# Kernel tuning notes

Measured on AMD Instinct MI355X. Metric: run time of the kernel, lower is better.

Reference implementation:

```python
import jax, jax.numpy as jnp
from jax import lax
import numpy as np

NUM_HEADS = 8
PATCH = 16
EPS_SUM = 1e-6


def resize_nearest(x, H, W):
    # torch F.interpolate(mode='nearest'): src = floor(dst * in / out)
    ih, iw = x.shape[-2], x.shape[-1]
    ri = (jnp.arange(H) * ih) // H
    ci = (jnp.arange(W) * iw) // W
    return x[:, :, ri][:, :, :, ci]


def single_scale(x, delta, wq, bq, ws, bs):
    # x: [1+K, C, H, W]; delta: [K, 1, H0, W0]
    q, s = x[:1], x[1:]
    K, C, H, W = s.shape
    d = C // NUM_HEADS
    P = PATCH
    Hp, Wp = H // P, W // P
    S = P * P
    delta = resize_nearest(delta, H, W)  # [K,1,H,W]

    qf = jnp.transpose(q, (0, 2, 3, 1))[0] @ wq.T + bq            # [H,W,C]
    qh = qf.reshape(H, W, NUM_HEADS, d).transpose(2, 0, 1, 3)     # [h,H,W,d]
    sf = jnp.transpose(s, (0, 2, 3, 1)) @ ws.T + bs               # [K,H,W,C]
    sh = sf.reshape(K, H, W, NUM_HEADS, d).transpose(0, 3, 1, 2, 4)  # [K,h,H,W,d]

    fg = delta.reshape(K, P, Hp, P, Wp).transpose(0, 1, 3, 2, 4).reshape(K, S, Hp * Wp)
    bg = 1.0 - fg
    fg_sum = jnp.maximum(fg.sum(-1), EPS_SUM)  # [K,S]
    bg_sum = jnp.maximum(bg.sum(-1), EPS_SUM)

    sp = sh.reshape(K, NUM_HEADS, P, Hp, P, Wp, d).transpose(0, 1, 2, 4, 3, 5, 6)
    sp = sp.reshape(K, NUM_HEADS, S, Hp * Wp, d)  # [K,h,S,l,d]

    c_fg = jnp.einsum('ksl,khsld->khsd', fg, sp) / fg_sum[:, None, :, None]
    c_bg = jnp.einsum('ksl,khsld->khsd', bg, sp) / bg_sum[:, None, :, None]
    # concat along prototype dim then flatten as [h, K*2S, d] (K-major, fg-then-bg)
    c_s = jnp.concatenate([c_fg, c_bg], axis=2).transpose(1, 0, 2, 3).reshape(NUM_HEADS, K * 2 * S, d)
    v = jnp.concatenate([jnp.ones((K, S), c_s.dtype), jnp.zeros((K, S), c_s.dtype)], axis=1).reshape(-1)  # [K*2S]

    mask = jnp.concatenate([
        jnp.where(fg_sum < 1.0, -jnp.inf, 0.0),
        jnp.where(bg_sum < 1.0, -jnp.inf, 0.0)], axis=1).reshape(-1)  # [K*2S]

    attn = jnp.einsum('hyxd,hsd->hyxs', qh, c_s) + mask  # [h,H,W,K*2S]
    attn = jax.nn.softmax(attn, axis=-1)
    out = jnp.einsum('hyxs,s->hyx', attn, v)  # [h,H,W]
    return out.mean(0)[None, None]  # [1,1,H,W]


def group_norm(x, gamma, beta, groups=4, eps=1e-5):
    N, C, H, W = x.shape
    xr = x.reshape(N, groups, C // groups, H, W)
    mu = xr.mean((2, 3, 4), keepdims=True)
    var = xr.var((2, 3, 4), keepdims=True)
    xr = (xr - mu) * lax.rsqrt(var + eps)
    return xr.reshape(N, C, H, W) * gamma[None, :, None, None] + beta[None, :, None, None]


def conv2d(x, w, b, pad):
    y = lax.conv_general_dilated(x, w, (1, 1), [(pad, pad), (pad, pad)],
                                 dimension_numbers=('NCHW', 'OIHW', 'NCHW'))
    return y + b[None, :, None, None]


def setup_inputs() -> dict:
    key = jax.random.key(0)
    ks = jax.random.split(key, 24)
    K, C, H, W = 5, 256, 64, 64
    inp = {}
    for i in range(4):
        inp[f'x{i}'] = jax.random.normal(ks[i], (1 + K, C, H, W), jnp.float32)
    inp['delta_onehot_x'] = jax.random.randint(ks[4], (K, 1, 256, 256), 0, 2).astype(jnp.float32)
    inp['wq'] = jax.random.normal(ks[5], (C, C), jnp.float32) * 0.02
    inp['bq'] = jnp.zeros((C,), jnp.float32)
    inp['ws'] = jax.random.normal(ks[6], (C, C), jnp.float32) * 0.02
    inp['bs'] = jnp.zeros((C,), jnp.float32)
    inp['cw1'] = jax.random.normal(ks[7], (16, 4, 5, 5), jnp.float32) * 0.05
    inp['cb1'] = jnp.zeros((16,), jnp.float32)
    inp['g1'] = jnp.ones((16,), jnp.float32)
    inp['be1'] = jnp.zeros((16,), jnp.float32)
    inp['cw2'] = jax.random.normal(ks[8], (64, 16, 5, 5), jnp.float32) * 0.05
    inp['cb2'] = jnp.zeros((64,), jnp.float32)
    inp['g2'] = jnp.ones((64,), jnp.float32)
    inp['be2'] = jnp.zeros((64,), jnp.float32)
    inp['cw3'] = jax.random.normal(ks[9], (128, 64, 3, 3), jnp.float32) * 0.05
    inp['cb3'] = jnp.zeros((128,), jnp.float32)
    inp['g3'] = jnp.ones((128,), jnp.float32)
    inp['be3'] = jnp.zeros((128,), jnp.float32)
    return inp


def reference(x0, x1, x2, x3, delta_onehot_x, wq, bq, ws, bs,
              cw1, cb1, g1, be1, cw2, cb2, g2, be2, cw3, cb3, g3, be3):
    masks = [single_scale(x, delta_onehot_x, wq, bq, ws, bs) for x in (x0, x1, x2, x3)]
    cm = jnp.concatenate(masks, axis=1)  # [1, nlayers=4, H, W]
    # idx=1 conv head: kernels [5,5,3], channels [16,64,128], GroupNorm(4)+ReLU
    h = jax.nn.relu(group_norm(conv2d(cm, cw1, cb1, 2), g1, be1))
    h = jax.nn.relu(group_norm(conv2d(h, cw2, cb2, 2), g2, be2))
    h = jax.nn.relu(group_norm(conv2d(h, cw3, cb3, 1), g3, be3))
    return h
```

## Files before the change

kernel.cpp:

```cpp
#include <hip/hip_runtime.h>
#include <hip/hip_bf16.h>
#include <stdint.h>

#define CCH 256
#define NPIX 4096
#define NH 8
#define M2 2560
#define LOG2E 1.44269504088896f
#define GN_NB 32

typedef __attribute__((ext_vector_type(8))) short short8;
typedef __attribute__((ext_vector_type(4))) float f32x4;

__device__ __forceinline__ uint16_t f2bfu(float f) {
    uint32_t u = __builtin_bit_cast(uint32_t, f);
    return (uint16_t)((u + 0x7FFFu + ((u >> 16) & 1u)) >> 16);
}
__device__ __forceinline__ uint32_t pack_bf2(float a, float b) {
    return (uint32_t)f2bfu(a) | ((uint32_t)f2bfu(b) << 16);
}
__device__ __forceinline__ short8 u4_to_s8(uint4 v) {
    return __builtin_bit_cast(short8, v);
}

__device__ __forceinline__ void prep_w_one(const float* __restrict__ w, uint16_t* __restrict__ Wk,
                                           int idx, int Cin, int Cout, int K2) {
    int kk = idx & 31;
    int oc = (idx >> 5) % Cout;
    int ck = idx / (32 * Cout);
    int k = ck * 32 + kk;
    int tap = k / Cin, ic = k % Cin;
    float v = (tap < K2) ? w[((size_t)oc * Cin + ic) * K2 + tap] : 0.0f;
    Wk[idx] = f2bfu(v);
}

__global__ void prep_all(const float* __restrict__ wq, const float* __restrict__ wsm,
                         const float* __restrict__ cw1, const float* __restrict__ cw2,
                         const float* __restrict__ cw3,
                         uint16_t* __restrict__ WB, uint16_t* __restrict__ Wk1,
                         uint16_t* __restrict__ Wk2, uint16_t* __restrict__ Wk3) {
    int idx = blockIdx.x * 256 + threadIdx.x;
    if (idx < 131072) {
        const float* src = (idx < 65536) ? wq : wsm;
        WB[idx] = f2bfu(src[idx & 65535]);
        return;
    }
    idx -= 131072;
    if (idx < 2048)  { prep_w_one(cw1, Wk1, idx, 4, 16, 25);  return; }
    idx -= 2048;
    if (idx < 26624) { prep_w_one(cw2, Wk2, idx, 16, 64, 25); return; }
    idx -= 26624;
    if (idx < 73728) { prep_w_one(cw3, Wk3, idx, 64, 128, 9); return; }
}

__global__ __launch_bounds__(256) void patch_sum(
        const float* __restrict__ x0, const float* __restrict__ x1,
        const float* __restrict__ x2, const float* __restrict__ x3,
        const float* __restrict__ dox, uint16_t* __restrict__ PS,
        float* __restrict__ inv, float* __restrict__ mexpb) {
    int z = blockIdx.z;
    int sc = z / 5, k = z % 5;
    const float* xim = ((sc == 0) ? x0 : (sc == 1) ? x1 : (sc == 2) ? x2 : x3)
                       + (size_t)(k + 1) * CCH * NPIX;
    int p1 = blockIdx.x, chq = blockIdx.y;
    int tid = threadIdx.x;
    int cloc = tid >> 6, col = tid & 63;
    __shared__ float wls[4][64];
    __shared__ uint16_t pst[2][16][72];
    wls[cloc][col] = dox[(size_t)k * 65536 + (size_t)(16 * p1 + 4 * cloc) * 256 + 4 * col];
    __syncthreads();
    float w0 = wls[0][col], w1 = wls[1][col], w2 = wls[2][col], w3 = wls[3][col];
    const float* xbase = xim + p1 * 256 + col;
#pragma unroll 4
    for (int it = 0; it < 16; ++it) {
        int c = chq * 64 + it * 4 + cloc;
        const float* xp = xbase + (size_t)c * NPIX;
        float v0 = xp[0], v1 = xp[64], v2 = xp[128], v3 = xp[192];
        float pf = w0 * v0 + w1 * v1 + w2 * v2 + w3 * v3;
        float pb = (v0 + v1 + v2 + v3) - pf;
        pf += __shfl_xor(pf, 1); pf += __shfl_xor(pf, 2);
        pb += __shfl_xor(pb, 1); pb += __shfl_xor(pb, 2);
        if ((col & 3) == 0) {
            int q = col >> 2, cl = it * 4 + cloc;
            pst[0][q][cl] = f2bfu(pf);
            pst[1][q][cl] = f2bfu(pb);
        }
    }
    if (chq == 0 && tid < 64) {
        float ws = w0 + w1 + w2 + w3;
        ws += __shfl_xor(ws, 1); ws += __shfl_xor(ws, 2);
        if ((col & 3) == 0) {
            int s = p1 * 16 + (col >> 2);
            float fsum = ws, bsum = 16.f - ws;
            int mf = k * 512 + s, mbk = mf + 256;
            mexpb[sc * M2 + mf]  = (fsum < 1.f) ? 0.f : 1.f;
            mexpb[sc * M2 + mbk] = (bsum < 1.f) ? 0.f : 1.f;
            inv[(size_t)(z * 2 + 0) * 256 + s] = 1.f / fmaxf(fsum, 1e-6f);
            inv[(size_t)(z * 2 + 1) * 256 + s] = 1.f / fmaxf(bsum, 1e-6f);
        }
    }
    __syncthreads();
    int fb = tid >> 7, rem = tid & 127;
    int q = rem >> 3, chunk = rem & 7;
    uint4 v = *(const uint4*)&pst[fb][q][chunk * 8];
    int s = p1 * 16 + q;
    *(uint4*)&PS[((size_t)(z * 2 + fb) * 256 + s) * CCH + chq * 64 + chunk * 8] = v;
}

__global__ __launch_bounds__(256) void cent_gemm(
        const uint16_t* __restrict__ PS, const uint16_t* __restrict__ WB,
        const float* __restrict__ bs, const float* __restrict__ inv,
        uint16_t* __restrict__ Csbf) {
    int tid = threadIdx.x, lane = tid & 63, wid = tid >> 6;
    int lp = lane & 15, g = lane >> 4;
    int rowb = blockIdx.x * 128 + wid * 32;
    int cob = blockIdx.y * 64;
    const uint16_t* wsb = WB + 65536;
    f32x4 acc[2][4] = {};
#pragma unroll
    for (int ks = 0; ks < 8; ++ks) {
        int k0 = ks * 32;
        uint4 a0 = *(const uint4*)(PS + (size_t)(rowb + lp) * CCH + k0 + g * 8);
        uint4 a1 = *(const uint4*)(PS + (size_t)(rowb + 16 + lp) * CCH + k0 + g * 8);
        short8 af[2] = {u4_to_s8(a0), u4_to_s8(a1)};
        short8 b[4];
#pragma unroll
        for (int t = 0; t < 4; ++t) {
            uint4 bw = *(const uint4*)(wsb + (size_t)(cob + t * 16 + lp) * 256 + k0 + g * 8);
            b[t] = u4_to_s8(bw);
        }
#pragma unroll
        for (int m = 0; m < 2; ++m)
#pragma unroll
            for (int t = 0; t < 4; ++t)
                acc[m][t] = __builtin_amdgcn_mfma_f32_16x16x32_bf16(af[m], b[t], acc[m][t], 0, 0, 0);
    }
#pragma unroll
    for (int m = 0; m < 2; ++m)
#pragma unroll
        for (int t = 0; t < 4; ++t) {
            int co = cob + t * 16 + lp;
            int h = co >> 5, d = co & 31;
            float bv = bs[co];
#pragma unroll
            for (int r = 0; r < 4; ++r) {
                int row = rowb + m * 16 + g * 4 + r;
                int zz = row >> 9, fb = (row >> 8) & 1, s = row & 255;
                int scc = zz / 5, kk = zz % 5;
                int slot = kk * 512 + fb * 256 + s;
                float val = acc[m][t][r] * inv[row] + bv;
                Csbf[(((size_t)scc * NH + h) * M2 + slot) * 32 + d] = f2bfu(val);
            }
        }
}

__global__ __launch_bounds__(512) void q_gemm(
        const float* __restrict__ x0, const float* __restrict__ x1,
        const float* __restrict__ x2, const float* __restrict__ x3,
        const uint16_t* __restrict__ WB, const float* __restrict__ bq,
        uint16_t* __restrict__ Qbf) {
    int sc = blockIdx.y;
    const float* xim = (sc == 0) ? x0 : (sc == 1) ? x1 : (sc == 2) ? x2 : x3;
    int p0 = blockIdx.x * 64;
    int tid = threadIdx.x, lane = tid & 63, wid = tid >> 6;
    int lp = lane & 15, g = lane >> 4;
    int wm = wid >> 1, wn = wid & 1;
    __shared__ uint32_t Al[16][68];
    f32x4 acc[8] = {};
#pragma unroll
    for (int ks = 0; ks < 8; ++ks) {
        int k0 = ks * 32;
        __syncthreads();
        if (tid < 256) {
            int rp = tid >> 4, f4i = tid & 15;
            float4 v0 = *(const float4*)(xim + (size_t)(k0 + 2 * rp) * NPIX + p0 + f4i * 4);
            float4 v1 = *(const float4*)(xim + (size_t)(k0 + 2 * rp + 1) * NPIX + p0 + f4i * 4);
            *(uint4*)&Al[rp][f4i * 4] = make_uint4(
                pack_bf2(v0.x, v1.x), pack_bf2(v0.y, v1.y),
                pack_bf2(v0.z, v1.z), pack_bf2(v0.w, v1.w));
        }
        __syncthreads();
        short8 b[8];
#pragma unroll
        for (int tn = 0; tn < 8; ++tn) {
            uint4 bw = *(const uint4*)(WB + (size_t)(wn * 128 + tn * 16 + lp) * 256 + k0 + g * 8);
            b[tn] = u4_to_s8(bw);
        }
        int px = wm * 16 + lp;
        uint4 av = make_uint4(Al[4 * g + 0][px], Al[4 * g + 1][px],
                              Al[4 * g + 2][px], Al[4 * g + 3][px]);
        short8 af = u4_to_s8(av);
#pragma unroll
        for (int tn = 0; tn < 8; ++tn)
            acc[tn] = __builtin_amdgcn_mfma_f32_16x16x32_bf16(af, b[tn], acc[tn], 0, 0, 0);
    }
#pragma unroll
    for (int tn = 0; tn < 8; ++tn) {
        int co = wn * 128 + tn * 16 + lp;
        float bv = bq[co];
#pragma unroll
        for (int r = 0; r < 4; ++r) {
            int row = p0 + wm * 16 + g * 4 + r;
            Qbf[((size_t)(sc * NPIX + row)) * CCH + co] = f2bfu((acc[tn][r] + bv) * LOG2E);
        }
    }
}

__global__ __launch_bounds__(256) void attn_v6(
        const uint16_t* __restrict__ Qbf, const uint16_t* __restrict__ Csbf,
        const float* __restrict__ mexpb, float* __restrict__ sfbuf) {
    int head = blockIdx.y;
    int sc = blockIdx.z >> 2, split = blockIdx.z & 3;
    int tid = threadIdx.x;
    int lane = tid & 63, wid = tid >> 6;
    int lp = lane & 15, g = lane >> 4;
    int p0w = blockIdx.x * 256 + wid * 64;

    const uint16_t* Qs = Qbf + (size_t)sc * NPIX * CCH;
    const uint16_t* csb = Csbf + ((size_t)sc * NH + head) * M2 * 32;
    const float* mb = mexpb + sc * M2;

    short8 aq[4];
#pragma unroll
    for (int m = 0; m < 4; m++) {
        uint4 qv = *(const uint4*)(Qs + (size_t)(p0w + m * 16 + lp) * CCH + head * 32 + g * 8);
        aq[m] = u4_to_s8(qv);
    }

    const f32x4 zero4 = {0.f, 0.f, 0.f, 0.f};
    float sfg[4][4] = {}, sbg[4][4] = {};
    int cbeg = split * 640;
    for (int c0loc = 0; c0loc < 640; c0loc += 64) {
        int c0 = cbeg + c0loc;
        bool fg = ((c0 & 511) < 256);
        short8 bf[4];
        float mexp[4];
#pragma unroll
        for (int t = 0; t < 4; t++) {
            int row = c0 + t * 16 + lp;
            bf[t] = u4_to_s8(*(const uint4*)(csb + (size_t)row * 32 + g * 8));
            mexp[t] = mb[row];
        }
        if (fg) {
#pragma unroll
            for (int m = 0; m < 4; m++)
#pragma unroll
                for (int t = 0; t < 4; t++) {
                    f32x4 c = __builtin_amdgcn_mfma_f32_16x16x32_bf16(aq[m], bf[t], zero4, 0, 0, 0);
#pragma unroll
                    for (int r = 0; r < 4; r++)
                        sfg[m][r] = fmaf(__builtin_amdgcn_exp2f(c[r]), mexp[t], sfg[m][r]);
                }
        } else {
#pragma unroll
            for (int m = 0; m < 4; m++)
#pragma unroll
                for (int t = 0; t < 4; t++) {
                    f32x4 c = __builtin_amdgcn_mfma_f32_16x16x32_bf16(aq[m], bf[t], zero4, 0, 0, 0);
#pragma unroll
                    for (int r = 0; r < 4; r++)
                        sbg[m][r] = fmaf(__builtin_amdgcn_exp2f(c[r]), mexp[t], sbg[m][r]);
                }
        }
    }
#pragma unroll
    for (int m = 0; m < 4; m++)
#pragma unroll
        for (int r = 0; r < 4; r++) {
#pragma unroll
            for (int msk = 1; msk < 16; msk <<= 1) {
                sfg[m][r] += __shfl_xor(sfg[m][r], msk);
                sbg[m][r] += __shfl_xor(sbg[m][r], msk);
            }
        }
    if (lp == 0) {
        float* sf = sfbuf + (size_t)((sc * 4 + split) * 2) * NH * NPIX;
        float* so = sf + (size_t)head * NPIX;
        float* fo = sf + (size_t)(NH + head) * NPIX;
#pragma unroll
        for (int m = 0; m < 4; m++)
#pragma unroll
            for (int r = 0; r < 4; r++) {
                int px = p0w + m * 16 + g * 4 + r;
                so[px] = sfg[m][r] + sbg[m][r];
                fo[px] = sfg[m][r];
            }
    }
}

__global__ void mean_heads3(const float* __restrict__ sfbuf, float* __restrict__ cm) {
    int idx = blockIdx.x * 256 + threadIdx.x;
    int sc = idx >> 12, p = idx & 4095;
    const float* b = sfbuf + (size_t)sc * 4 * 2 * NH * NPIX;
    float acc = 0.f;
#pragma unroll
    for (int h = 0; h < NH; h++) {
        float sv = 0.f, fv = 0.f;
#pragma unroll
        for (int sp = 0; sp < 4; sp++) {
            sv += b[((size_t)(sp * 2) * NH + h) * NPIX + p];
            fv += b[((size_t)(sp * 2 + 1) * NH + h) * NPIX + p];
        }
        acc += fv / sv;
    }
    cm[idx] = 0.125f * acc;
}

template<int CIN, int COUT, int KSZ>
__global__ __launch_bounds__(256) void conv_mfma(
        const float* __restrict__ in, const uint16_t* __restrict__ Wk,
        const float* __restrict__ bias, float* __restrict__ out) {
    constexpr int PAD = KSZ / 2;
    constexpr int NTAP = KSZ * KSZ;
    constexpr int K = CIN * NTAP;
    constexpr int CK = (K + 31) / 32;
    constexpr int PXP = 64 + 2 * PAD;
    constexpr int ICB = (CIN >= 8) ? CIN / 8 : 1;
    __shared__ uint16_t Xs[KSZ * PXP * CIN];
    int tid = threadIdx.x;
    int lane = tid & 63, wv = tid >> 6;
    int lp = lane & 15, g = lane >> 4;
    int y = blockIdx.x;
    int oc0 = blockIdx.y * 64;

    if (CIN >= 8) {
        for (int idx = tid; idx < KSZ * ICB * PXP; idx += 256) {
            int pxp = idx % PXP; int rem = idx / PXP;
            int icb = rem % ICB; int r = rem / ICB;
            int gy = y + r - PAD, gx = pxp - PAD;
            bool ok = ((unsigned)gy < 64u) && ((unsigned)gx < 64u);
            const float* ip = in + (size_t)(icb * 8) * NPIX + gy * 64 + gx;
            uint32_t wb[4];
#pragma unroll
            for (int j = 0; j < 4; j++) {
                float v0 = ok ? ip[(size_t)(2 * j) * NPIX] : 0.f;
                float v1 = ok ? ip[(size_t)(2 * j + 1) * NPIX] : 0.f;
                wb[j] = pack_bf2(v0, v1);
            }
            *(uint4*)&Xs[(size_t)idx * 8] = make_uint4(wb[0], wb[1], wb[2], wb[3]);
        }
    } else {
        for (int idx = tid; idx < KSZ * PXP; idx += 256) {
            int pxp = idx % PXP; int r = idx / PXP;
            int gy = y + r - PAD, gx = pxp - PAD;
            bool ok = ((unsigned)gy < 64u) && ((unsigned)gx < 64u);
            const float* ip = in + (size_t)gy * 64 + gx;
            float v0 = ok ? ip[0] : 0.f, v1 = ok ? ip[NPIX] : 0.f;
            float v2 = ok ? ip[2 * NPIX] : 0.f, v3 = ok ? ip[3 * NPIX] : 0.f;
            *(uint2*)&Xs[(size_t)idx * 4] = make_uint2(pack_bf2(v0, v1), pack_bf2(v2, v3));
        }
    }
    __syncthreads();

    int tmb, tme, tn;
    if (COUT >= 64) { tn = wv; tmb = 0; tme = 4; }
    else            { tn = 0;  tmb = wv; tme = wv + 1; }
    int oc = oc0 + tn * 16 + lp;
    f32x4 acc[4] = {};

#pragma unroll
    for (int ck = 0; ck < CK; ck++) {
        const uint16_t* wp = Wk + ((size_t)ck * COUT + oc) * 32 + g * 8;
        uint4 bw = *(const uint4*)wp;
        short8 bfr = u4_to_s8(bw);
        if (CIN >= 8) {
            int gk = ck * 4 + g;
            int tap = gk / ICB; if (tap > NTAP - 1) tap = NTAP - 1;
            int icb = gk % ICB;
            int r = tap / KSZ, dx = tap % KSZ;
            int base = (r * ICB + icb) * PXP * 8;
            for (int tm = tmb; tm < tme; tm++) {
                int pxp = tm * 16 + lp + dx;
                uint4 av = *(const uint4*)&Xs[base + pxp * 8];
                short8 afr = u4_to_s8(av);
                acc[tm] = __builtin_amdgcn_mfma_f32_16x16x32_bf16(afr, bfr, acc[tm], 0, 0, 0);
            }
        } else {
            int gk = ck * 4 + g;
            int t0 = 2 * gk;     if (t0 > NTAP - 1) t0 = NTAP - 1;
            int t1 = 2 * gk + 1; if (t1 > NTAP - 1) t1 = NTAP - 1;
            int r0 = t0 / KSZ, dx0 = t0 % KSZ;
            int r1 = t1 / KSZ, dx1 = t1 % KSZ;
            for (int tm = tmb; tm < tme; tm++) {
                uint2 a0 = *(const uint2*)&Xs[((size_t)(r0 * PXP + tm * 16 + lp + dx0)) * 4];
                uint2 a1 = *(const uint2*)&Xs[((size_t)(r1 * PXP + tm * 16 + lp + dx1)) * 4];
                uint4 av = make_uint4(a0.x, a0.y, a1.x, a1.y);
                short8 afr = u4_to_s8(av);
                acc[tm] = __builtin_amdgcn_mfma_f32_16x16x32_bf16(afr, bfr, acc[tm], 0, 0, 0);
            }
        }
    }
    float bv = bias[oc];
    for (int tm = tmb; tm < tme; tm++)
#pragma unroll
        for (int r = 0; r < 4; r++) {
            int px = tm * 16 + g * 4 + r;
            out[(size_t)oc * NPIX + y * 64 + px] = acc[tm][r] + bv;
        }
}

__global__ __launch_bounds__(256) void gn_part(const float* __restrict__ in, int Cg,
                                               float* __restrict__ part) {
    int g = blockIdx.x, b = blockIdx.y;
    int n4 = Cg * 1024;
    const float4* base = (const float4*)(in + (size_t)g * Cg * NPIX);
    float s = 0.0f, s2 = 0.0f;
    for (int i = b * 256 + threadIdx.x; i < n4; i += GN_NB * 256) {
        float4 v = base[i];
        s += v.x + v.y + v.z + v.w;
        s2 = fmaf(v.x, v.x, s2); s2 = fmaf(v.y, v.y, s2);
        s2 = fmaf(v.z, v.z, s2); s2 = fmaf(v.w, v.w, s2);
    }
#pragma unroll
    for (int off = 32; off; off >>= 1) {
        s += __shfl_down(s, off);
        s2 += __shfl_down(s2, off);
    }
    __shared__ float rs[4], rs2[4];
    int w = threadIdx.x >> 6;
    if ((threadIdx.x & 63) == 0) { rs[w] = s; rs2[w] = s2; }
    __syncthreads();
    if (threadIdx.x == 0) {
        part[(g * GN_NB + b) * 2]     = rs[0] + rs[1] + rs[2] + rs[3];
        part[(g * GN_NB + b) * 2 + 1] = rs2[0] + rs2[1] + rs2[2] + rs2[3];
    }
}

__global__ __launch_bounds__(256) void gn_apply_relu(const float* __restrict__ in, const float* __restrict__ part,
                                                     const float* __restrict__ gamma, const float* __restrict__ beta,
                                                     int Cg, float* __restrict__ out) {
    int idx4 = blockIdx.x * 256 + threadIdx.x;
    int c = idx4 >> 10;
    int g = c / Cg;
    float s = 0.0f, s2 = 0.0f;
#pragma unroll
    for (int b = 0; b < GN_NB; b++) {
        s  += part[(g * GN_NB + b) * 2];
        s2 += part[(g * GN_NB + b) * 2 + 1];
    }
    float n = (float)(Cg * NPIX);
    float mu = s / n;
    float rstd = rsqrtf(s2 / n - mu * mu + 1e-5f);
    float ga = gamma[c] * rstd;
    float be = beta[c] - mu * ga;
    float4 v = ((const float4*)in)[idx4];
    float4 o;
    o.x = fmaf(v.x, ga, be); o.x = o.x > 0.f ? o.x : 0.f;
    o.y = fmaf(v.y, ga, be); o.y = o.y > 0.f ? o.y : 0.f;
    o.z = fmaf(v.z, ga, be); o.z = o.z > 0.f ? o.z : 0.f;
    o.w = fmaf(v.w, ga, be); o.w = o.w > 0.f ? o.w : 0.f;
    ((float4*)out)[idx4] = o;
}

extern "C" void kernel_launch(void* const* d_in, const int* in_sizes, int n_in,
                              void* d_out, int out_size, void* d_ws, size_t ws_size,
                              hipStream_t stream) {
    const float* x0 = (const float*)d_in[0];
    const float* x1 = (const float*)d_in[1];
    const float* x2 = (const float*)d_in[2];
    const float* x3 = (const float*)d_in[3];
    const float* dox = (const float*)d_in[4];
    const float* wq  = (const float*)d_in[5];
    const float* bq  = (const float*)d_in[6];
    const float* wsm = (const float*)d_in[7];
    const float* bs  = (const float*)d_in[8];
    const float* cw1 = (const float*)d_in[9];
    const float* cb1 = (const float*)d_in[10];
    const float* g1  = (const float*)d_in[11];
    const float* be1 = (const float*)d_in[12];
    const float* cw2 = (const float*)d_in[13];
    const float* cb2 = (const float*)d_in[14];
    const float* g2  = (const float*)d_in[15];
    const float* be2 = (const float*)d_in[16];
    const float* cw3 = (const float*)d_in[17];
    const float* cb3 = (const float*)d_in[18];
    const float* g3  = (const float*)d_in[19];
    const float* be3 = (const float*)d_in[20];

    uint16_t* Qbf  = (uint16_t*)d_ws;
    uint16_t* Csbf = Qbf + (size_t)4194304;
    uint16_t* PS   = Csbf + (size_t)2621440;
    uint16_t* WB   = PS + (size_t)2621440;
    uint16_t* Wk1  = WB + 131072;
    uint16_t* Wk2  = Wk1 + 2048;
    uint16_t* Wk3  = Wk2 + 26624;
    float* fbase  = (float*)(Wk3 + 73728);
    float* mexpb  = fbase;
    float* inv    = mexpb + 10240;
    float* sfbuf  = inv + 10240;
    float* cm     = sfbuf + 1048576;
    float* h1     = cm + 16384;
    float* h2     = h1 + 65536;
    float* h3     = h2 + 262144;
    float* gnpart = h3 + 524288;

    prep_all<<<(233472 + 255) / 256, 256, 0, stream>>>(wq, wsm, cw1, cw2, cw3, WB, Wk1, Wk2, Wk3);

    patch_sum<<<dim3(16, 4, 20), 256, 0, stream>>>(x0, x1, x2, x3, dox, PS, inv, mexpb);
    q_gemm<<<dim3(64, 4), 512, 0, stream>>>(x0, x1, x2, x3, WB, bq, Qbf);
    cent_gemm<<<dim3(80, 4), 256, 0, stream>>>(PS, WB, bs, inv, Csbf);
    attn_v6<<<dim3(16, NH, 16), 256, 0, stream>>>(Qbf, Csbf, mexpb, sfbuf);
    mean_heads3<<<64, 256, 0, stream>>>(sfbuf, cm);

    conv_mfma<4, 16, 5><<<dim3(64, 1), 256, 0, stream>>>(cm, Wk1, cb1, h1);
    gn_part<<<dim3(4, GN_NB), 256, 0, stream>>>(h1, 4, gnpart);
    gn_apply_relu<<<(16 * 1024) / 256, 256, 0, stream>>>(h1, gnpart, g1, be1, 4, h1);

    conv_mfma<16, 64, 5><<<dim3(64, 1), 256, 0, stream>>>(h1, Wk2, cb2, h2);
    gn_part<<<dim3(4, GN_NB), 256, 0, stream>>>(h2, 16, gnpart);
    gn_apply_relu<<<(64 * 1024) / 256, 256, 0, stream>>>(h2, gnpart, g2, be2, 16, h2);

    conv_mfma<64, 128, 3><<<dim3(64, 2), 256, 0, stream>>>(h2, Wk3, cb3, h3);
    gn_part<<<dim3(4, GN_NB), 256, 0, stream>>>(h3, 32, gnpart);
    gn_apply_relu<<<(128 * 1024) / 256, 256, 0, stream>>>(h3, gnpart, g3, be3, 32, (float*)d_out);
}
```

Measured before the change: 147.2 us.

## Stage centroid tiles through double-buffered swizzled LDS in attention kernel

The attention kernel now loads each 64-row centroid tile cooperatively into shared memory, with each thread fetching one 16-byte chunk, and double-buffers it. The next tile's global load is issued before the current tile's MFMA and exp work. Previously all four waves read the same centroid rows straight from global or L2. The LDS layout uses an XOR swizzle to avoid bank conflicts, at the cost of a __syncthreads per iteration.

```diff
diff --git a/kernel.cpp b/kernel.cpp
--- a/kernel.cpp
+++ b/kernel.cpp
@@ -206,7 +206,7 @@
     }
 }
 
-__global__ __launch_bounds__(256) void attn_v6(
+__global__ __launch_bounds__(256) void attn_v7(
         const uint16_t* __restrict__ Qbf, const uint16_t* __restrict__ Csbf,
         const float* __restrict__ mexpb, float* __restrict__ sfbuf) {
     int head = blockIdx.y;
@@ -216,6 +216,8 @@
     int lp = lane & 15, g = lane >> 4;
     int p0w = blockIdx.x * 256 + wid * 64;
 
+    __shared__ uint16_t Cl[2][2048];
+
     const uint16_t* Qs = Qbf + (size_t)sc * NPIX * CCH;
     const uint16_t* csb = Csbf + ((size_t)sc * NH + head) * M2 * 32;
     const float* mb = mexpb + sc * M2;
@@ -227,19 +229,35 @@
         aq[m] = u4_to_s8(qv);
     }
 
+    int sr = tid >> 2, sq4 = tid & 3;
+    int ssw = sq4 ^ (sr & 3);
+    int cbeg = split * 640;
+    const uint16_t* sgp = csb + ((size_t)(cbeg + sr)) * 32 + ssw * 8;
+    const int ldst_off = sr * 32 + sq4 * 8;
+
     const f32x4 zero4 = {0.f, 0.f, 0.f, 0.f};
     float sfg[4][4] = {}, sbg[4][4] = {};
-    int cbeg = split * 640;
-    for (int c0loc = 0; c0loc < 640; c0loc += 64) {
-        int c0 = cbeg + c0loc;
+
+    {
+        uint4 gv = *(const uint4*)sgp;
+        *(uint4*)(&Cl[0][ldst_off]) = gv;
+    }
+    __syncthreads();
+
+    for (int ci = 0; ci < 10; ci++) {
+        int c0 = cbeg + ci * 64;
         bool fg = ((c0 & 511) < 256);
+        uint4 ngv;
+        if (ci < 9) ngv = *(const uint4*)(sgp + (size_t)(ci + 1) * 64 * 32);
+
+        const uint16_t* lbuf = &Cl[ci & 1][0];
         short8 bf[4];
         float mexp[4];
 #pragma unroll
         for (int t = 0; t < 4; t++) {
-            int row = c0 + t * 16 + lp;
-            bf[t] = u4_to_s8(*(const uint4*)(csb + (size_t)row * 32 + g * 8));
-            mexp[t] = mb[row];
+            int r = t * 16 + lp;
+            bf[t] = u4_to_s8(*(const uint4*)(lbuf + r * 32 + ((g ^ (lp & 3)) * 8)));
+            mexp[t] = mb[c0 + r];
         }
         if (fg) {
 #pragma unroll
@@ -262,6 +280,10 @@
                         sbg[m][r] = fmaf(__builtin_amdgcn_exp2f(c[r]), mexp[t], sbg[m][r]);
                 }
         }
+        if (ci < 9) {
+            *(uint4*)(&Cl[(ci + 1) & 1][ldst_off]) = ngv;
+        }
+        __syncthreads();
     }
 #pragma unroll
     for (int m = 0; m < 4; m++)
@@ -499,7 +521,7 @@
     patch_sum<<<dim3(16, 4, 20), 256, 0, stream>>>(x0, x1, x2, x3, dox, PS, inv, mexpb);
     q_gemm<<<dim3(64, 4), 512, 0, stream>>>(x0, x1, x2, x3, WB, bq, Qbf);
     cent_gemm<<<dim3(80, 4), 256, 0, stream>>>(PS, WB, bs, inv, Csbf);
-    attn_v6<<<dim3(16, NH, 16), 256, 0, stream>>>(Qbf, Csbf, mexpb, sfbuf);
+    attn_v7<<<dim3(16, NH, 16), 256, 0, stream>>>(Qbf, Csbf, mexpb, sfbuf);
     mean_heads3<<<64, 256, 0, stream>>>(sfbuf, cm);
 
     conv_mfma<4, 16, 5><<<dim3(64, 1), 256, 0, stream>>>(cm, Wk1, cb1, h1);
```

Result: faster. 144.4 us (-2.0%).

## Fuse GroupNorm statistics into conv epilogue and GN apply into next conv's load

Applied to the files above, without the earlier changes.

The conv epilogue now reduces per-group partial sums and sums of squares, and the next conv applies GroupNorm and ReLU while staging its input tile into shared memory. This removes two gn_part launches and two gn_apply_relu launches along with the extra full read and write of the intermediate activations. The cost is a small per-block reduction of partials and more per-element work during the input staging. The final layer still uses a separate gn_apply_relu.

```diff
diff --git a/kernel.cpp b/kernel.cpp
--- a/kernel.cpp
+++ b/kernel.cpp
@@ -7,7 +7,6 @@
 #define NH 8
 #define M2 2560
 #define LOG2E 1.44269504088896f
-#define GN_NB 32
 
 typedef __attribute__((ext_vector_type(8))) short short8;
 typedef __attribute__((ext_vector_type(4))) float f32x4;
@@ -306,10 +305,13 @@
     cm[idx] = 0.125f * acc;
 }
 
-template<int CIN, int COUT, int KSZ>
+template<int CIN, int COUT, int KSZ, int NPIN, int NPOUT, bool GNIN>
 __global__ __launch_bounds__(256) void conv_mfma(
         const float* __restrict__ in, const uint16_t* __restrict__ Wk,
-        const float* __restrict__ bias, float* __restrict__ out) {
+        const float* __restrict__ bias,
+        const float* __restrict__ gin, const float* __restrict__ bein,
+        const float2* __restrict__ pin,
+        float* __restrict__ out, float2* __restrict__ pout) {
     constexpr int PAD = KSZ / 2;
     constexpr int NTAP = KSZ * KSZ;
     constexpr int K = CIN * NTAP;
@@ -317,11 +319,37 @@
     constexpr int PXP = 64 + 2 * PAD;
     constexpr int ICB = (CIN >= 8) ? CIN / 8 : 1;
     __shared__ uint16_t Xs[KSZ * PXP * CIN];
+    __shared__ float gaL[CIN], beL[CIN];
+    __shared__ float gmu[4], grs[4];
     int tid = threadIdx.x;
     int lane = tid & 63, wv = tid >> 6;
     int lp = lane & 15, g = lane >> 4;
     int y = blockIdx.x;
     int oc0 = blockIdx.y * 64;
+
+    if (GNIN) {
+        float s = 0.f, s2 = 0.f;
+        for (int i = lane; i < NPIN; i += 64) {
+            float2 p = pin[wv * NPIN + i];
+            s += p.x; s2 += p.y;
+        }
+#pragma unroll
+        for (int m = 32; m; m >>= 1) { s += __shfl_xor(s, m); s2 += __shfl_xor(s2, m); }
+        if (lane == 0) {
+            float n = (float)((CIN / 4) * NPIX);
+            float mu = s / n;
+            gmu[wv] = mu;
+            grs[wv] = rsqrtf(s2 / n - mu * mu + 1e-5f);
+        }
+        __syncthreads();
+        if (tid < CIN) {
+            int gg = tid / (CIN / 4);
+            float ga = gin[tid] * grs[gg];
+            gaL[tid] = ga;
+            beL[tid] = bein[tid] - gmu[gg] * ga;
+        }
+        __syncthreads();
+    }
 
     if (CIN >= 8) {
         for (int idx = tid; idx < KSZ * ICB * PXP; idx += 256) {
@@ -333,8 +361,14 @@
             uint32_t wb[4];
 #pragma unroll
             for (int j = 0; j < 4; j++) {
+                int c0c = icb * 8 + 2 * j, c1c = c0c + 1;
                 float v0 = ok ? ip[(size_t)(2 * j) * NPIX] : 0.f;
                 float v1 = ok ? ip[(size_t)(2 * j + 1) * NPIX] : 0.f;
+                if (GNIN) {
+                    v0 = fmaf(v0, gaL[c0c], beL[c0c]); v0 = v0 > 0.f ? v0 : 0.f;
+                    v1 = fmaf(v1, gaL[c1c], beL[c1c]); v1 = v1 > 0.f ? v1 : 0.f;
+                    if (!ok) { v0 = 0.f; v1 = 0.f; }
+                }
                 wb[j] = pack_bf2(v0, v1);
             }
             *(uint4*)&Xs[(size_t)idx * 8] = make_uint4(wb[0], wb[1], wb[2], wb[3]);
@@ -391,52 +425,46 @@
         }
     }
     float bv = bias[oc];
+    float ps = 0.f, ps2 = 0.f;
     for (int tm = tmb; tm < tme; tm++)
 #pragma unroll
         for (int r = 0; r < 4; r++) {
             int px = tm * 16 + g * 4 + r;
-            out[(size_t)oc * NPIX + y * 64 + px] = acc[tm][r] + bv;
-        }
-}
-
-__global__ __launch_bounds__(256) void gn_part(const float* __restrict__ in, int Cg,
-                                               float* __restrict__ part) {
-    int g = blockIdx.x, b = blockIdx.y;
-    int n4 = Cg * 1024;
-    const float4* base = (const float4*)(in + (size_t)g * Cg * NPIX);
-    float s = 0.0f, s2 = 0.0f;
-    for (int i = b * 256 + threadIdx.x; i < n4; i += GN_NB * 256) {
-        float4 v = base[i];
-        s += v.x + v.y + v.z + v.w;
-        s2 = fmaf(v.x, v.x, s2); s2 = fmaf(v.y, v.y, s2);
-        s2 = fmaf(v.z, v.z, s2); s2 = fmaf(v.w, v.w, s2);
-    }
-#pragma unroll
-    for (int off = 32; off; off >>= 1) {
-        s += __shfl_down(s, off);
-        s2 += __shfl_down(s2, off);
-    }
-    __shared__ float rs[4], rs2[4];
-    int w = threadIdx.x >> 6;
-    if ((threadIdx.x & 63) == 0) { rs[w] = s; rs2[w] = s2; }
-    __syncthreads();
-    if (threadIdx.x == 0) {
-        part[(g * GN_NB + b) * 2]     = rs[0] + rs[1] + rs[2] + rs[3];
-        part[(g * GN_NB + b) * 2 + 1] = rs2[0] + rs2[1] + rs2[2] + rs2[3];
-    }
-}
-
-__global__ __launch_bounds__(256) void gn_apply_relu(const float* __restrict__ in, const float* __restrict__ part,
+            float val = acc[tm][r] + bv;
+            out[(size_t)oc * NPIX + y * 64 + px] = val;
+            ps += val;
+            ps2 = fmaf(val, val, ps2);
+        }
+    if (COUT >= 64) {
+#pragma unroll
+        for (int m = 32; m; m >>= 1) { ps += __shfl_xor(ps, m); ps2 += __shfl_xor(ps2, m); }
+        if (lane == 0) {
+            if (COUT == 64) {
+                pout[wv * NPOUT + y] = make_float2(ps, ps2);
+            } else {
+                int grp = blockIdx.y * 2 + (wv >> 1);
+                pout[grp * NPOUT + y * 2 + (wv & 1)] = make_float2(ps, ps2);
+            }
+        }
+    } else {
+#pragma unroll
+        for (int m : {1, 2, 16, 32}) { ps += __shfl_xor(ps, m); ps2 += __shfl_xor(ps2, m); }
+        int q = (lane >> 2) & 3;
+        if (lane == q * 4)
+            pout[q * NPOUT + y * 4 + wv] = make_float2(ps, ps2);
+    }
+}
+
+__global__ __launch_bounds__(256) void gn_apply_relu(const float* __restrict__ in, const float2* __restrict__ part,
                                                      const float* __restrict__ gamma, const float* __restrict__ beta,
-                                                     int Cg, float* __restrict__ out) {
+                                                     int Cg, int npart, float* __restrict__ out) {
     int idx4 = blockIdx.x * 256 + threadIdx.x;
     int c = idx4 >> 10;
     int g = c / Cg;
     float s = 0.0f, s2 = 0.0f;
-#pragma unroll
-    for (int b = 0; b < GN_NB; b++) {
-        s  += part[(g * GN_NB + b) * 2];
-        s2 += part[(g * GN_NB + b) * 2 + 1];
+    for (int b = 0; b < npart; b++) {
+        float2 p = part[g * npart + b];
+        s += p.x; s2 += p.y;
     }
     float n = (float)(Cg * NPIX);
     float mu = s / n;
@@ -492,7 +520,9 @@
     float* h1     = cm + 16384;
     float* h2     = h1 + 65536;
     float* h3     = h2 + 262144;
-    float* gnpart = h3 + 524288;
+    float2* part1 = (float2*)(h3 + 524288);
+    float2* part2 = part1 + 4 * 256;
+    float2* part3 = part2 + 4 * 64;
 
     prep_all<<<(233472 + 255) / 256, 256, 0, stream>>>(wq, wsm, cw1, cw2, cw3, WB, Wk1, Wk2, Wk3);
 
@@ -502,15 +532,11 @@
     attn_v6<<<dim3(16, NH, 16), 256, 0, stream>>>(Qbf, Csbf, mexpb, sfbuf);
     mean_heads3<<<64, 256, 0, stream>>>(sfbuf, cm);
 
-    conv_mfma<4, 16, 5><<<dim3(64, 1), 256, 0, stream>>>(cm, Wk1, cb1, h1);
-    gn_part<<<dim3(4, GN_NB), 256, 0, stream>>>(h1, 4, gnpart);
-    gn_apply_relu<<<(16 * 1024) / 256, 256, 0, stream>>>(h1, gnpart, g1, be1, 4, h1);
-
-    conv_mfma<16, 64, 5><<<dim3(64, 1), 256, 0, stream>>>(h1, Wk2, cb2, h2);
-    gn_part<<<dim3(4, GN_NB), 256, 0, stream>>>(h2, 16, gnpart);
-    gn_apply_relu<<<(64 * 1024) / 256, 256, 0, stream>>>(h2, gnpart, g2, be2, 16, h2);
-
-    conv_mfma<64, 128, 3><<<dim3(64, 2), 256, 0, stream>>>(h2, Wk3, cb3, h3);
-    gn_part<<<dim3(4, GN_NB), 256, 0, stream>>>(h3, 32, gnpart);
-    gn_apply_relu<<<(128 * 1024) / 256, 256, 0, stream>>>(h3, gnpart, g3, be3, 32, (float*)d_out);
-}
+    conv_mfma<4, 16, 5, 1, 256, false><<<dim3(64, 1), 256, 0, stream>>>(
+        cm, Wk1, cb1, nullptr, nullptr, nullptr, h1, part1);
+    conv_mfma<16, 64, 5, 256, 64, true><<<dim3(64, 1), 256, 0, stream>>>(
+        h1, Wk2, cb2, g1, be1, part1, h2, part2);
+    conv_mfma<64, 128, 3, 64, 128, true><<<dim3(64, 2), 256, 0, stream>>>(
+        h2, Wk3, cb3, g2, be2, part2, h3, part3);
+    gn_apply_relu<<<(128 * 1024) / 256, 256, 0, stream>>>(h3, part3, g3, be3, 32, 128, (float*)d_out);
+}
```

After: 144.6 us (median of 2 runs). Within noise of the previous version (-1.8%).
